# Kernel optimization log

Hardware: AMD Instinct MI355X
Metric: run time of the kernel (lower is better)

## Reference

```python
import jax, jax.numpy as jnp
import numpy as np

N, E = 20000, 320000
NF, EF = 4, 4
HID, HEADS, MODEL_HID = 128, 4, 128


def _p(key, shape, scale=0.1):
    return scale * jax.random.normal(key, shape, dtype=jnp.float32)


def setup_inputs() -> dict:
    key = jax.random.key(0)
    ks = jax.random.split(key, 32)
    x = jax.random.normal(ks[0], (N, NF), dtype=jnp.float32)
    src = jax.random.randint(ks[1], (E,), 0, N)
    off = jax.random.randint(ks[2], (E,), 1, N)
    dst = (src + off) % N  # no self-loops (PyG removes then re-adds them)
    edge_index = jnp.stack([src, dst]).astype(jnp.int64)
    edge_attr = jax.random.uniform(ks[3], (E, EF), dtype=jnp.float32)
    d = dict(x=x, edge_index=edge_index, edge_attr=edge_attr)
    # input_proj
    d['Wp'] = _p(ks[4], (NF, HID)); d['bp'] = jnp.zeros((HID,), jnp.float32)
    # GAT layer 1: in=HID, heads=HEADS, out=HID, concat
    d['W1'] = _p(ks[5], (HID, HEADS * HID)); d['We1'] = _p(ks[6], (EF, HEADS * HID))
    d['as1'] = _p(ks[7], (HEADS, HID)); d['ad1'] = _p(ks[8], (HEADS, HID)); d['ae1'] = _p(ks[9], (HEADS, HID))
    d['b1'] = jnp.zeros((HEADS * HID,), jnp.float32)
    d['g1'] = jnp.ones((HEADS * HID,), jnp.float32); d['be1'] = jnp.zeros((HEADS * HID,), jnp.float32)
    # GAT layer 2: in=HEADS*HID, heads=1, out=HID, mean
    d['W2'] = _p(ks[10], (HEADS * HID, HID)); d['We2'] = _p(ks[11], (EF, HID))
    d['as2'] = _p(ks[12], (1, HID)); d['ad2'] = _p(ks[13], (1, HID)); d['ae2'] = _p(ks[14], (1, HID))
    d['b2'] = jnp.zeros((HID,), jnp.float32)
    d['g2'] = jnp.ones((HID,), jnp.float32); d['be2'] = jnp.zeros((HID,), jnp.float32)
    # output proj + importance scorer
    d['Wo'] = _p(ks[15], (HID, MODEL_HID)); d['bo'] = jnp.zeros((MODEL_HID,), jnp.float32)
    d['Wi'] = _p(ks[16], (MODEL_HID, 1)); d['bi'] = jnp.zeros((1,), jnp.float32)
    return d


def _layer_norm(x, g, b, eps=1e-5):
    mu = x.mean(-1, keepdims=True)
    v = ((x - mu) ** 2).mean(-1, keepdims=True)
    return (x - mu) * jax.lax.rsqrt(v + eps) * g + b


def _segment_softmax(logits, seg, num):
    m = jax.ops.segment_max(logits, seg, num_segments=num)
    e = jnp.exp(logits - m[seg])
    d = jax.ops.segment_sum(e, seg, num_segments=num)
    return e / d[seg]


def _forward(x, edge_index, edge_attr, Wp, bp, W1, We1, as1, ad1, ae1, b1, g1, be1,
             W2, We2, as2, ad2, ae2, b2, g2, be2, Wo, bo, Wi, bi):
    n = x.shape[0]
    src, dst = edge_index[0], edge_index[1]
    e = edge_attr.shape[0]
    # add_self_loops with fill_value='mean': self-loop attr = mean of incoming edge_attr
    deg = jax.ops.segment_sum(jnp.ones((e,), edge_attr.dtype), dst, num_segments=n)
    loop_attr = jax.ops.segment_sum(edge_attr, dst, num_segments=n) / jnp.maximum(deg, 1.0)[:, None]
    loops = jnp.arange(n)
    src_f = jnp.concatenate([src, loops])
    dst_f = jnp.concatenate([dst, loops])
    ea = jnp.concatenate([edge_attr, loop_attr], axis=0)  # [E+N, EF]

    def gat(h, W, We, a_s, a_d, a_e, bias, heads, out_c, concat):
        xh = (h @ W).reshape(n, heads, out_c)                 # [N,H,C]
        eh = (ea @ We).reshape(-1, heads, out_c)              # [E+N,H,C]
        al_s = (xh * a_s).sum(-1)                             # [N,H]
        al_d = (xh * a_d).sum(-1)                             # [N,H]
        al_e = (eh * a_e).sum(-1)                             # [E+N,H]
        logits = jax.nn.leaky_relu(al_s[src_f] + al_d[dst_f] + al_e, negative_slope=0.2)
        alpha = _segment_softmax(logits, dst_f, n)            # [E+N,H]
        out = jax.ops.segment_sum(xh[src_f] * alpha[..., None], dst_f, num_segments=n)
        out = out.reshape(n, heads * out_c) if concat else out.mean(axis=1)
        return out + bias, alpha

    h = x @ Wp + bp
    h, _ = gat(h, W1, We1, as1, ad1, ae1, b1, HEADS, HID, True)
    h = jax.nn.elu(_layer_norm(h, g1, be1))  # dropout is a no-op in eval
    h, edge_attention = gat(h, W2, We2, as2, ad2, ae2, b2, 1, HID, False)
    h = _layer_norm(h, g2, be2)
    emb = h @ Wo + bo
    importance = jax.nn.sigmoid(emb @ Wi + bi).squeeze(-1)
    return emb, edge_attention, importance


def reference(x, edge_index, edge_attr, Wp, bp, W1, We1, as1, ad1, ae1, b1, g1, be1,
              W2, We2, as2, ad2, ae2, b2, g2, be2, Wo, bo, Wi, bi):
    return _forward(x, edge_index, edge_attr, Wp, bp, W1, We1, as1, ad1, ae1, b1, g1, be1,
                    W2, We2, as2, ad2, ae2, b2, g2, be2, Wo, bo, Wi, bi)
```

## Files before the change

kernel.cpp:

```cpp
#include <hip/hip_runtime.h>
#include <math.h>
#include <stdint.h>

#define N_NODES 20000
#define N_EDGES 320000
#define EN_TOT  340000
#define CAP     160

typedef __attribute__((ext_vector_type(8))) _Float16 half8v;
typedef __attribute__((ext_vector_type(2))) _Float16 half2v;
typedef __attribute__((ext_vector_type(4))) float float4v;

__device__ __forceinline__ ushort f2h(float f) {
    _Float16 h = (_Float16)f;
    return __builtin_bit_cast(ushort, h);
}
__device__ __forceinline__ float h2f(ushort s) {
    return (float)__builtin_bit_cast(_Float16, s);
}

__global__ void k_deg(const int* __restrict__ dst, int* __restrict__ degi) {
    int e = blockIdx.x * 256 + threadIdx.x;
    if (e >= N_EDGES) return;
    atomicAdd(&degi[dst[e]], 1);
}

__global__ __launch_bounds__(1024) void k_scan(const int* __restrict__ degi, int* __restrict__ offsets,
                                               const float* __restrict__ We1, const float* __restrict__ ae1,
                                               const float* __restrict__ We2, const float* __restrict__ ae2,
                                               float* __restrict__ M1, float* __restrict__ m2) {
    __shared__ int s[1024];
    int t = threadIdx.x;
    int n0 = t * 20;
    int tot = 0;
    for (int i = 0; i < 20; i++) {
        int n = n0 + i;
        if (n < N_NODES) tot += degi[n] + 1;
    }
    s[t] = tot;
    __syncthreads();
    for (int off = 1; off < 1024; off <<= 1) {
        int v = (t >= off) ? s[t - off] : 0;
        __syncthreads();
        s[t] += v;
        __syncthreads();
    }
    int run = s[t] - tot;
    for (int i = 0; i < 20; i++) {
        int n = n0 + i;
        if (n < N_NODES) {
            offsets[n] = run;
            run += degi[n] + 1;
        }
    }
    if (t == 1023) offsets[N_NODES] = s[1023];
    if (t < 16) {
        int f = t >> 2, h = t & 3;
        float acc = 0.f;
        for (int c = 0; c < 128; c++) acc += We1[f * 512 + h * 128 + c] * ae1[h * 128 + c];
        M1[f * 4 + h] = acc;
    } else if (t < 20) {
        int f = t - 16;
        float acc = 0.f;
        for (int c = 0; c < 128; c++) acc += We2[f * 128 + c] * ae2[c];
        m2[f] = acc;
    }
}

__global__ void k_fill(const int* __restrict__ src, const int* __restrict__ dst,
                       const int* __restrict__ offsets, int* __restrict__ cursor,
                       int2* __restrict__ csr_se) {
    int i = blockIdx.x * 256 + threadIdx.x;
    if (i >= EN_TOT) return;
    int d, sidx, eid;
    if (i < N_EDGES) { d = dst[i]; sidx = src[i]; eid = i; }
    else { int n = i - N_EDGES; d = n; sidx = n; eid = N_EDGES + n; }
    int pos = offsets[d] + atomicAdd(&cursor[d], 1);
    csr_se[pos] = make_int2(sidx, eid);
}

__global__ __launch_bounds__(256) void k_misc(const int* __restrict__ offsets, const int2* __restrict__ csr_se,
                                              const float* __restrict__ eattr, float* __restrict__ loopattr,
                                              const float* __restrict__ W1, const float* __restrict__ W2,
                                              const float* __restrict__ Wo, ushort* __restrict__ W1T,
                                              ushort* __restrict__ W2T, ushort* __restrict__ WoT,
                                              const float* __restrict__ x, const float* __restrict__ Wp,
                                              const float* __restrict__ bp, ushort* __restrict__ h0h) {
    int b = blockIdx.x;
    int tid = threadIdx.x;
    if (b < 5000) {
        int wv = tid >> 6, l = tid & 63;
        int n = b * 4 + wv;
        if (n >= N_NODES) return;
        int start = offsets[n], end = offsets[n + 1];
        float sx = 0.f, sy = 0.f, sz = 0.f, sw = 0.f;
        for (int p = start + l; p < end; p += 64) {
            int eid = csr_se[p].y;
            if (eid < N_EDGES) {
                float4 e = *(const float4*)&eattr[(size_t)eid * 4];
                sx += e.x; sy += e.y; sz += e.z; sw += e.w;
            }
        }
        for (int off = 32; off; off >>= 1) {
            sx += __shfl_down(sx, off);
            sy += __shfl_down(sy, off);
            sz += __shfl_down(sz, off);
            sw += __shfl_down(sw, off);
        }
        if (l == 0) {
            float inv = 1.0f / fmaxf((float)(end - start - 1), 1.0f);
            float4 o;
            o.x = sx * inv; o.y = sy * inv; o.z = sz * inv; o.w = sw * inv;
            *(float4*)&loopattr[(size_t)n * 4] = o;
        }
    } else if (b < 5576) {
        int i = (b - 5000) * 256 + tid;
        if (i < 512 * 128) {
            int nn = i >> 7, kk = i & 127;
            W1T[i] = f2h(W1[kk * 512 + nn]);
        } else if (i < 2 * 512 * 128) {
            int j = i - 512 * 128;
            int nn = j >> 9, kk = j & 511;
            W2T[j] = f2h(W2[kk * 128 + nn]);
        } else if (i < 2 * 512 * 128 + 128 * 128) {
            int j = i - 2 * 512 * 128;
            int nn = j >> 7, kk = j & 127;
            WoT[j] = f2h(Wo[kk * 128 + nn]);
        }
    } else {
        int n = (b - 5576) * 2 + (tid >> 7);
        int c = tid & 127;
        float acc = bp[c];
#pragma unroll
        for (int f = 0; f < 4; f++) acc += x[n * 4 + f] * Wp[f * 128 + c];
        h0h[(size_t)n * 128 + c] = f2h(acc);
    }
}

__global__ __launch_bounds__(256) void k_gemm_hf(const ushort* __restrict__ A, const ushort* __restrict__ BT,
                                                 float* __restrict__ Cf, ushort* __restrict__ Ch,
                                                 int M, int Nn, int K, const float* __restrict__ bias,
                                                 const float* __restrict__ asv, const float* __restrict__ adv,
                                                 float* __restrict__ outS, float* __restrict__ outD,
                                                 int hstride, const float* __restrict__ sbias) {
    __shared__ ushort As[64 * 64];
    __shared__ ushort Bs[128 * 64];
    __shared__ float redS[4][64];
    __shared__ float redD[4][64];
    const int tid = threadIdx.x;
    const int lane = tid & 63, wid = tid >> 6;
    const int m0 = blockIdx.x * 64, n0 = blockIdx.y * 128;
    float4v acc[4][2];
#pragma unroll
    for (int i = 0; i < 4; i++)
#pragma unroll
        for (int j = 0; j < 2; j++) acc[i][j] = (float4v){0.f, 0.f, 0.f, 0.f};

    for (int k0 = 0; k0 < K; k0 += 64) {
        __syncthreads();
#pragma unroll
        for (int i = 0; i < 2; i++) {
            int c = tid + i * 256;
            int row = c >> 3, sl = c & 7;
            int off = row * 128 + ((sl ^ (row & 7)) << 4);
            uint4 va = make_uint4(0u, 0u, 0u, 0u);
            if (m0 + row < M) va = *(const uint4*)&A[(size_t)(m0 + row) * K + k0 + sl * 8];
            *(uint4*)((char*)As + off) = va;
        }
#pragma unroll
        for (int i = 0; i < 4; i++) {
            int c = tid + i * 256;
            int row = c >> 3, sl = c & 7;
            int off = row * 128 + ((sl ^ (row & 7)) << 4);
            uint4 vb = *(const uint4*)&BT[(size_t)(n0 + row) * K + k0 + sl * 8];
            *(uint4*)((char*)Bs + off) = vb;
        }
        __syncthreads();
#pragma unroll
        for (int kk = 0; kk < 2; kk++) {
            half8v af[4], bq[2];
            int sl = kk * 4 + (lane >> 4);
#pragma unroll
            for (int mi = 0; mi < 4; mi++) {
                int row = (lane & 15) + mi * 16;
                af[mi] = *(const half8v*)((const char*)As + row * 128 + ((sl ^ (row & 7)) << 4));
            }
#pragma unroll
            for (int ni = 0; ni < 2; ni++) {
                int row = wid * 32 + ni * 16 + (lane & 15);
                bq[ni] = *(const half8v*)((const char*)Bs + row * 128 + ((sl ^ (row & 7)) << 4));
            }
#pragma unroll
            for (int mi = 0; mi < 4; mi++)
#pragma unroll
                for (int ni = 0; ni < 2; ni++)
                    acc[mi][ni] = __builtin_amdgcn_mfma_f32_16x16x32_f16(af[mi], bq[ni], acc[mi][ni], 0, 0, 0);
        }
    }
    float bcol[2];
#pragma unroll
    for (int ni = 0; ni < 2; ni++)
        bcol[ni] = bias ? bias[n0 + wid * 32 + ni * 16 + (lane & 15)] : 0.f;
#pragma unroll
    for (int mi = 0; mi < 4; mi++) {
#pragma unroll
        for (int j = 0; j < 4; j++) {
            int row = m0 + mi * 16 + ((lane >> 4) << 2) + j;
            if (row < M) {
#pragma unroll
                for (int ni = 0; ni < 2; ni++) {
                    int col = n0 + wid * 32 + ni * 16 + (lane & 15);
                    float v = acc[mi][ni][j] + bcol[ni];
                    if (Cf) Cf[(size_t)row * Nn + col] = v;
                    if (Ch) Ch[(size_t)row * Nn + col] = f2h(v);
                }
            }
        }
    }
    if (asv) {
        float asl[2], adl[2];
#pragma unroll
        for (int ni = 0; ni < 2; ni++) {
            int col = n0 + wid * 32 + ni * 16 + (lane & 15);
            asl[ni] = asv[col];
            adl[ni] = adv ? adv[col] : 0.f;
        }
        float psv[4][4], pdv[4][4];
#pragma unroll
        for (int mi = 0; mi < 4; mi++)
#pragma unroll
            for (int j = 0; j < 4; j++) {
                float v0 = acc[mi][0][j] + bcol[0];
                float v1 = acc[mi][1][j] + bcol[1];
                psv[mi][j] = v0 * asl[0] + v1 * asl[1];
                pdv[mi][j] = v0 * adl[0] + v1 * adl[1];
            }
#pragma unroll
        for (int off = 1; off < 16; off <<= 1) {
#pragma unroll
            for (int mi = 0; mi < 4; mi++)
#pragma unroll
                for (int j = 0; j < 4; j++) {
                    psv[mi][j] += __shfl_xor(psv[mi][j], off);
                    pdv[mi][j] += __shfl_xor(pdv[mi][j], off);
                }
        }
        if ((lane & 15) == 0) {
#pragma unroll
            for (int mi = 0; mi < 4; mi++)
#pragma unroll
                for (int j = 0; j < 4; j++) {
                    int r = mi * 16 + ((lane >> 4) << 2) + j;
                    redS[wid][r] = psv[mi][j];
                    redD[wid][r] = pdv[mi][j];
                }
        }
        __syncthreads();
        if (tid < 64) {
            int row = m0 + tid;
            if (row < M) {
                float ss = redS[0][tid] + redS[1][tid] + redS[2][tid] + redS[3][tid];
                float dd = redD[0][tid] + redD[1][tid] + redD[2][tid] + redD[3][tid];
                if (sbias) {
                    outS[row] = 1.0f / (1.0f + __expf(-(ss + sbias[0])));
                } else {
                    outS[row * hstride + blockIdx.y] = ss;
                    if (outD) outD[row * hstride + blockIdx.y] = dd;
                }
            }
        }
    }
}

__global__ __launch_bounds__(128) void k_agg1(const int* __restrict__ offsets, const int2* __restrict__ csr_se,
                                              const float* __restrict__ eattr, const float* __restrict__ loopattr,
                                              const float* __restrict__ als, const float* __restrict__ aldv,
                                              const float* __restrict__ M1, const ushort* __restrict__ xhh,
                                              const float* __restrict__ b1, const float* __restrict__ g1,
                                              const float* __restrict__ be1, ushort* __restrict__ h1h) {
    int wv = threadIdx.x >> 6, lane = threadIdx.x & 63;
    int n = blockIdx.x * 2 + wv;
    __shared__ float Lc[2][CAP][4];
    __shared__ int   sSrc[2][CAP];
    __shared__ float mhs[2][4], shs[2][4];

    int start = offsets[n];
    int cnt = offsets[n + 1] - start;

    int hh = lane & 3;
    float aldn = aldv[n * 4 + hh];
    float c0 = M1[hh], c1 = M1[4 + hh], c2 = M1[8 + hh], c3 = M1[12 + hh];
    float m = -1e30f, s = 0.f;
    for (int j = lane >> 2; j < cnt; j += 16) {
        int2 se = csr_se[start + j];
        const float* eap = (se.y < N_EDGES) ? &eattr[(size_t)se.y * 4] : &loopattr[(size_t)(se.y - N_EDGES) * 4];
        float4 e4 = *(const float4*)eap;
        float l = als[se.x * 4 + hh] + aldn + e4.x * c0 + e4.y * c1 + e4.z * c2 + e4.w * c3;
        l = (l >= 0.f) ? l : 0.2f * l;
        Lc[wv][j][hh] = l;
        if (hh == 0) sSrc[wv][j] = se.x;
        float mn = fmaxf(m, l);
        s = s * __expf(m - mn) + __expf(l - mn);
        m = mn;
    }
#pragma unroll
    for (int off = 4; off < 64; off <<= 1) {
        float mo = __shfl_xor(m, off), so = __shfl_xor(s, off);
        float mn = fmaxf(m, mo);
        s = s * __expf(m - mn) + so * __expf(mo - mn);
        m = mn;
    }
    if (lane < 4) { mhs[wv][lane] = m; shs[wv][lane] = 1.0f / s; }

    int tot = cnt * 4;
    for (int idx = lane; idx < tot; idx += 64) {
        int j = idx >> 2, h = idx & 3;
        Lc[wv][j][h] = __expf(Lc[wv][j][h] - mhs[wv][h]) * shs[wv][h];
    }

    half2v hac0 = (half2v)0, hac1 = (half2v)0, hac2 = (half2v)0, hac3 = (half2v)0;
    int hg = lane >> 4;
    uint ch = (uint)lane * 8u;
    int j = 0;
    for (; j + 8 <= cnt; j += 8) {
        _Float16 av[8];
        uint4 vv[8];
#pragma unroll
        for (int t = 0; t < 8; t++) av[t] = (_Float16)Lc[wv][j + t][hg];
#pragma unroll
        for (int t = 0; t < 8; t++) vv[t] = *(const uint4*)&xhh[((uint)sSrc[wv][j + t] << 9) + ch];
#pragma unroll
        for (int t = 0; t < 8; t++) {
            half2v a2 = (half2v){av[t], av[t]};
            const half2v* pv = (const half2v*)&vv[t];
            hac0 = pv[0] * a2 + hac0;
            hac1 = pv[1] * a2 + hac1;
            hac2 = pv[2] * a2 + hac2;
            hac3 = pv[3] * a2 + hac3;
        }
    }
    for (; j < cnt; j++) {
        _Float16 a = (_Float16)Lc[wv][j][hg];
        half2v a2 = (half2v){a, a};
        uint4 v = *(const uint4*)&xhh[((uint)sSrc[wv][j] << 9) + ch];
        const half2v* pv = (const half2v*)&v;
        hac0 = pv[0] * a2 + hac0;
        hac1 = pv[1] * a2 + hac1;
        hac2 = pv[2] * a2 + hac2;
        hac3 = pv[3] * a2 + hac3;
    }

    float4 ba = *(const float4*)&b1[ch];
    float4 bb = *(const float4*)&b1[ch + 4];
    float v0 = (float)hac0[0] + ba.x, v1 = (float)hac0[1] + ba.y;
    float v2 = (float)hac1[0] + ba.z, v3 = (float)hac1[1] + ba.w;
    float v4 = (float)hac2[0] + bb.x, v5 = (float)hac2[1] + bb.y;
    float v6 = (float)hac3[0] + bb.z, v7 = (float)hac3[1] + bb.w;
    float s8 = v0 + v1 + v2 + v3 + v4 + v5 + v6 + v7;
#pragma unroll
    for (int off = 1; off < 64; off <<= 1) s8 += __shfl_xor(s8, off);
    float mu = s8 * (1.0f / 512.0f);
    float d0 = v0 - mu, d1 = v1 - mu, d2 = v2 - mu, d3 = v3 - mu;
    float d4 = v4 - mu, d5 = v5 - mu, d6 = v6 - mu, d7 = v7 - mu;
    float sq = d0 * d0 + d1 * d1 + d2 * d2 + d3 * d3 + d4 * d4 + d5 * d5 + d6 * d6 + d7 * d7;
#pragma unroll
    for (int off = 1; off < 64; off <<= 1) sq += __shfl_xor(sq, off);
    float rstd = rsqrtf(sq * (1.0f / 512.0f) + 1e-5f);
    float4 ga = *(const float4*)&g1[ch];
    float4 gb = *(const float4*)&g1[ch + 4];
    float4 ea = *(const float4*)&be1[ch];
    float4 eb = *(const float4*)&be1[ch + 4];
    float y0 = d0 * rstd * ga.x + ea.x, y1 = d1 * rstd * ga.y + ea.y;
    float y2 = d2 * rstd * ga.z + ea.z, y3 = d3 * rstd * ga.w + ea.w;
    float y4 = d4 * rstd * gb.x + eb.x, y5 = d5 * rstd * gb.y + eb.y;
    float y6 = d6 * rstd * gb.z + eb.z, y7 = d7 * rstd * gb.w + eb.w;
    y0 = (y0 > 0.f) ? y0 : (__expf(y0) - 1.0f);
    y1 = (y1 > 0.f) ? y1 : (__expf(y1) - 1.0f);
    y2 = (y2 > 0.f) ? y2 : (__expf(y2) - 1.0f);
    y3 = (y3 > 0.f) ? y3 : (__expf(y3) - 1.0f);
    y4 = (y4 > 0.f) ? y4 : (__expf(y4) - 1.0f);
    y5 = (y5 > 0.f) ? y5 : (__expf(y5) - 1.0f);
    y6 = (y6 > 0.f) ? y6 : (__expf(y6) - 1.0f);
    y7 = (y7 > 0.f) ? y7 : (__expf(y7) - 1.0f);
    uint4 o;
    o.x = (uint)f2h(y0) | ((uint)f2h(y1) << 16);
    o.y = (uint)f2h(y2) | ((uint)f2h(y3) << 16);
    o.z = (uint)f2h(y4) | ((uint)f2h(y5) << 16);
    o.w = (uint)f2h(y6) | ((uint)f2h(y7) << 16);
    *(uint4*)&h1h[(size_t)n * 512 + ch] = o;
}

__global__ __launch_bounds__(128) void k_agg2(const int* __restrict__ offsets, const int2* __restrict__ csr_se,
                                              const float* __restrict__ eattr, const float* __restrict__ loopattr,
                                              const float* __restrict__ als, const float* __restrict__ aldv,
                                              const float* __restrict__ m2v, const ushort* __restrict__ xh2h,
                                              const float* __restrict__ b2, const float* __restrict__ g2,
                                              const float* __restrict__ be2, float* __restrict__ eaout,
                                              ushort* __restrict__ h2h) {
    int wv = threadIdx.x >> 6, lane = threadIdx.x & 63;
    int n = blockIdx.x * 2 + wv;
    __shared__ float Lc[2][CAP];
    __shared__ int   sS[2][CAP];
    __shared__ int   sE[2][CAP];

    int start = offsets[n];
    int cnt = offsets[n + 1] - start;
    float aldn = aldv[n];
    float c0 = m2v[0], c1 = m2v[1], c2 = m2v[2], c3 = m2v[3];
    float m = -1e30f, s = 0.f;
    for (int j = lane; j < cnt; j += 64) {
        int2 se = csr_se[start + j];
        const float* eap = (se.y < N_EDGES) ? &eattr[(size_t)se.y * 4] : &loopattr[(size_t)(se.y - N_EDGES) * 4];
        float4 e4 = *(const float4*)eap;
        float l = als[se.x] + aldn + e4.x * c0 + e4.y * c1 + e4.z * c2 + e4.w * c3;
        l = (l >= 0.f) ? l : 0.2f * l;
        Lc[wv][j] = l; sS[wv][j] = se.x; sE[wv][j] = se.y;
        float mn = fmaxf(m, l);
        s = s * __expf(m - mn) + __expf(l - mn);
        m = mn;
    }
#pragma unroll
    for (int off = 1; off < 64; off <<= 1) {
        float mo = __shfl_xor(m, off), so = __shfl_xor(s, off);
        float mn = fmaxf(m, mo);
        s = s * __expf(m - mn) + so * __expf(mo - mn);
        m = mn;
    }
    float inv = 1.0f / s;
    for (int j = lane; j < cnt; j += 64) {
        float a = __expf(Lc[wv][j] - m) * inv;
        Lc[wv][j] = a;
        eaout[sE[wv][j]] = a;
    }
    half2v hac = (half2v)0;
    uint ch = (uint)lane * 2u;
    int j = 0;
    for (; j + 8 <= cnt; j += 8) {
        _Float16 av[8];
        uint vv[8];
#pragma unroll
        for (int t = 0; t < 8; t++) av[t] = (_Float16)Lc[wv][j + t];
#pragma unroll
        for (int t = 0; t < 8; t++) vv[t] = *(const uint*)&xh2h[((uint)sS[wv][j + t] << 7) + ch];
#pragma unroll
        for (int t = 0; t < 8; t++) {
            half2v a2 = (half2v){av[t], av[t]};
            half2v pv = __builtin_bit_cast(half2v, vv[t]);
            hac = pv * a2 + hac;
        }
    }
    for (; j < cnt; j++) {
        _Float16 a = (_Float16)Lc[wv][j];
        half2v a2 = (half2v){a, a};
        half2v pv = __builtin_bit_cast(half2v, *(const uint*)&xh2h[((uint)sS[wv][j] << 7) + ch]);
        hac = pv * a2 + hac;
    }
    float2 bb = *(const float2*)&b2[ch];
    float v0 = (float)hac[0] + bb.x, v1 = (float)hac[1] + bb.y;
    float s2 = v0 + v1;
#pragma unroll
    for (int off = 1; off < 64; off <<= 1) s2 += __shfl_xor(s2, off);
    float mu = s2 * (1.0f / 128.0f);
    float d0 = v0 - mu, d1 = v1 - mu;
    float q = d0 * d0 + d1 * d1;
#pragma unroll
    for (int off = 1; off < 64; off <<= 1) q += __shfl_xor(q, off);
    float rstd = rsqrtf(q * (1.0f / 128.0f) + 1e-5f);
    float2 gg = *(const float2*)&g2[ch];
    float2 ee = *(const float2*)&be2[ch];
    float y0 = d0 * rstd * gg.x + ee.x;
    float y1 = d1 * rstd * gg.y + ee.y;
    uint o = (uint)f2h(y0) | ((uint)f2h(y1) << 16);
    *(uint*)&h2h[(size_t)n * 128 + ch] = o;
}

extern "C" void kernel_launch(void* const* d_in, const int* in_sizes, int n_in,
                              void* d_out, int out_size, void* d_ws, size_t ws_size,
                              hipStream_t stream) {
    const float* x    = (const float*)d_in[0];
    const int*   eidx = (const int*)d_in[1];
    const float* eattr= (const float*)d_in[2];
    const float* Wp   = (const float*)d_in[3];
    const float* bp   = (const float*)d_in[4];
    const float* W1   = (const float*)d_in[5];
    const float* We1  = (const float*)d_in[6];
    const float* as1  = (const float*)d_in[7];
    const float* ad1  = (const float*)d_in[8];
    const float* ae1  = (const float*)d_in[9];
    const float* b1   = (const float*)d_in[10];
    const float* g1   = (const float*)d_in[11];
    const float* be1  = (const float*)d_in[12];
    const float* W2   = (const float*)d_in[13];
    const float* We2  = (const float*)d_in[14];
    const float* as2  = (const float*)d_in[15];
    const float* ad2  = (const float*)d_in[16];
    const float* ae2  = (const float*)d_in[17];
    const float* b2   = (const float*)d_in[18];
    const float* g2   = (const float*)d_in[19];
    const float* be2  = (const float*)d_in[20];
    const float* Wo   = (const float*)d_in[21];
    const float* bo   = (const float*)d_in[22];
    const float* Wi   = (const float*)d_in[23];
    const float* bi   = (const float*)d_in[24];

    const int* src = eidx;
    const int* dst = eidx + N_EDGES;

    float* emb_out = (float*)d_out;
    float* ea_out  = emb_out + (size_t)N_NODES * 128;
    float* imp_out = ea_out + EN_TOT;

    char* w = (char*)d_ws;
    auto alloc = [&](size_t bytes) -> void* { void* p = (void*)w; w += (bytes + 255) & ~(size_t)255; return p; };
    ushort* xhh    = (ushort*)alloc((size_t)N_NODES * 512 * 2);
    ushort* h1h    = (ushort*)alloc((size_t)N_NODES * 512 * 2);
    ushort* h0h    = (ushort*)alloc((size_t)N_NODES * 128 * 2);
    ushort* xh2h   = (ushort*)alloc((size_t)N_NODES * 128 * 2);
    ushort* h2h    = (ushort*)alloc((size_t)N_NODES * 128 * 2);
    ushort* W1T    = (ushort*)alloc((size_t)512 * 128 * 2);
    ushort* W2T    = (ushort*)alloc((size_t)128 * 512 * 2);
    ushort* WoT    = (ushort*)alloc((size_t)128 * 128 * 2);
    int2*  csr_se  = (int2*)alloc((size_t)EN_TOT * 8);
    int*   offsets = (int*)alloc((size_t)(N_NODES + 1) * 4);
    int*   cursor  = (int*)alloc((size_t)N_NODES * 4);
    int*   degi    = (int*)alloc((size_t)N_NODES * 4);
    float* loopat  = (float*)alloc((size_t)N_NODES * 4 * 4);
    float* als1v   = (float*)alloc((size_t)N_NODES * 4 * 4);
    float* ald1v   = (float*)alloc((size_t)N_NODES * 4 * 4);
    float* als2v   = (float*)alloc((size_t)N_NODES * 4);
    float* ald2v   = (float*)alloc((size_t)N_NODES * 4);
    float* M1      = (float*)alloc(32 * 4);
    float* m2      = M1 + 16;

    hipMemsetAsync(degi,   0, (size_t)N_NODES * 4, stream);
    hipMemsetAsync(cursor, 0, (size_t)N_NODES * 4, stream);

    k_deg<<<(N_EDGES + 255) / 256, 256, 0, stream>>>(dst, degi);
    k_scan<<<1, 1024, 0, stream>>>(degi, offsets, We1, ae1, We2, ae2, M1, m2);
    k_fill<<<(EN_TOT + 255) / 256, 256, 0, stream>>>(src, dst, offsets, cursor, csr_se);
    k_misc<<<15576, 256, 0, stream>>>(offsets, csr_se, eattr, loopat, W1, W2, Wo,
                                      W1T, W2T, WoT, x, Wp, bp, h0h);

    k_gemm_hf<<<dim3((N_NODES + 63) / 64, 4), 256, 0, stream>>>(h0h, W1T, nullptr, xhh,
                                                                N_NODES, 512, 128, nullptr,
                                                                as1, ad1, als1v, ald1v, 4, nullptr);
    k_agg1<<<N_NODES / 2, 128, 0, stream>>>(offsets, csr_se, eattr, loopat, als1v, ald1v, M1,
                                            xhh, b1, g1, be1, h1h);

    k_gemm_hf<<<dim3((N_NODES + 63) / 64, 1), 256, 0, stream>>>(h1h, W2T, nullptr, xh2h,
                                                                N_NODES, 128, 512, nullptr,
                                                                as2, ad2, als2v, ald2v, 1, nullptr);
    k_agg2<<<N_NODES / 2, 128, 0, stream>>>(offsets, csr_se, eattr, loopat, als2v, ald2v, m2,
                                            xh2h, b2, g2, be2, ea_out, h2h);

    k_gemm_hf<<<dim3((N_NODES + 63) / 64, 1), 256, 0, stream>>>(h2h, WoT, emb_out, nullptr,
                                                                N_NODES, 128, 128, bo,
                                                                Wi, nullptr, imp_out, nullptr, 1, bi);
}
```

Baseline: 207.1 us.

## Replace LDS edge staging with recompute and wave shuffles in GAT aggregation

Both aggregation kernels no longer cache per-edge logits and source indices in fixed-capacity shared arrays. Edges are processed in 64-wide chunks: the softmax statistics pass recomputes logits, then a second pass recomputes them, normalises, packs the attention weights into registers and broadcasts them with __shfl to all lanes for the gather-accumulate. Layer 1 now gives each lane all four heads of one edge instead of one head. This drops LDS use and its capacity limit (CAP=160), in exchange for reading the edge data and computing the logits twice and adding per-edge shuffle work.

Measured after the change: 214.8 us. 3.7% more time.

```diff
diff --git a/kernel.cpp b/kernel.cpp
--- a/kernel.cpp
+++ b/kernel.cpp
@@ -5,7 +5,6 @@
 #define N_NODES 20000
 #define N_EDGES 320000
 #define EN_TOT  340000
-#define CAP     160
 
 typedef __attribute__((ext_vector_type(8))) _Float16 half8v;
 typedef __attribute__((ext_vector_type(2))) _Float16 half2v;
@@ -18,6 +17,10 @@
 __device__ __forceinline__ float h2f(ushort s) {
     return (float)__builtin_bit_cast(_Float16, s);
 }
+
+#define ONL(mm, ss, ll) { float _mn = fmaxf(mm, ll); ss = ss * __expf(mm - _mn) + __expf(ll - _mn); mm = _mn; }
+#define MRG(mm, ss, off) { float _mo = __shfl_xor(mm, off), _so = __shfl_xor(ss, off); \
+                           float _mn = fmaxf(mm, _mo); ss = ss * __expf(mm - _mn) + _so * __expf(_mo - _mn); mm = _mn; }
 
 __global__ void k_deg(const int* __restrict__ dst, int* __restrict__ degi) {
     int e = blockIdx.x * 256 + threadIdx.x;
@@ -280,74 +283,109 @@
                                               const float* __restrict__ be1, ushort* __restrict__ h1h) {
     int wv = threadIdx.x >> 6, lane = threadIdx.x & 63;
     int n = blockIdx.x * 2 + wv;
-    __shared__ float Lc[2][CAP][4];
-    __shared__ int   sSrc[2][CAP];
-    __shared__ float mhs[2][4], shs[2][4];
-
     int start = offsets[n];
     int cnt = offsets[n + 1] - start;
 
-    int hh = lane & 3;
-    float aldn = aldv[n * 4 + hh];
-    float c0 = M1[hh], c1 = M1[4 + hh], c2 = M1[8 + hh], c3 = M1[12 + hh];
-    float m = -1e30f, s = 0.f;
-    for (int j = lane >> 2; j < cnt; j += 16) {
-        int2 se = csr_se[start + j];
-        const float* eap = (se.y < N_EDGES) ? &eattr[(size_t)se.y * 4] : &loopattr[(size_t)(se.y - N_EDGES) * 4];
-        float4 e4 = *(const float4*)eap;
-        float l = als[se.x * 4 + hh] + aldn + e4.x * c0 + e4.y * c1 + e4.z * c2 + e4.w * c3;
-        l = (l >= 0.f) ? l : 0.2f * l;
-        Lc[wv][j][hh] = l;
-        if (hh == 0) sSrc[wv][j] = se.x;
-        float mn = fmaxf(m, l);
-        s = s * __expf(m - mn) + __expf(l - mn);
-        m = mn;
-    }
-#pragma unroll
-    for (int off = 4; off < 64; off <<= 1) {
-        float mo = __shfl_xor(m, off), so = __shfl_xor(s, off);
-        float mn = fmaxf(m, mo);
-        s = s * __expf(m - mn) + so * __expf(mo - mn);
-        m = mn;
-    }
-    if (lane < 4) { mhs[wv][lane] = m; shs[wv][lane] = 1.0f / s; }
-
-    int tot = cnt * 4;
-    for (int idx = lane; idx < tot; idx += 64) {
-        int j = idx >> 2, h = idx & 3;
-        Lc[wv][j][h] = __expf(Lc[wv][j][h] - mhs[wv][h]) * shs[wv][h];
-    }
+    float4 aldn = *(const float4*)&aldv[n * 4];
+    float M00 = M1[0],  M01 = M1[1],  M02 = M1[2],  M03 = M1[3];
+    float M10 = M1[4],  M11 = M1[5],  M12 = M1[6],  M13 = M1[7];
+    float M20 = M1[8],  M21 = M1[9],  M22 = M1[10], M23 = M1[11];
+    float M30 = M1[12], M31 = M1[13], M32 = M1[14], M33 = M1[15];
+
+    float m0 = -1e30f, m1 = -1e30f, m2 = -1e30f, m3 = -1e30f;
+    float s0 = 0.f, s1 = 0.f, s2 = 0.f, s3 = 0.f;
+    for (int jb = 0; jb < cnt; jb += 64) {
+        int j = jb + lane;
+        if (j < cnt) {
+            int2 se = csr_se[start + j];
+            const float* eap = (se.y < N_EDGES) ? &eattr[(size_t)se.y * 4] : &loopattr[(size_t)(se.y - N_EDGES) * 4];
+            float4 e4 = *(const float4*)eap;
+            float4 a4 = *(const float4*)&als[se.x * 4];
+            float l0 = a4.x + aldn.x + e4.x * M00 + e4.y * M10 + e4.z * M20 + e4.w * M30;
+            float l1 = a4.y + aldn.y + e4.x * M01 + e4.y * M11 + e4.z * M21 + e4.w * M31;
+            float l2 = a4.z + aldn.z + e4.x * M02 + e4.y * M12 + e4.z * M22 + e4.w * M32;
+            float l3 = a4.w + aldn.w + e4.x * M03 + e4.y * M13 + e4.z * M23 + e4.w * M33;
+            l0 = (l0 >= 0.f) ? l0 : 0.2f * l0;
+            l1 = (l1 >= 0.f) ? l1 : 0.2f * l1;
+            l2 = (l2 >= 0.f) ? l2 : 0.2f * l2;
+            l3 = (l3 >= 0.f) ? l3 : 0.2f * l3;
+            ONL(m0, s0, l0); ONL(m1, s1, l1); ONL(m2, s2, l2); ONL(m3, s3, l3);
+        }
+    }
+#pragma unroll
+    for (int off = 1; off < 64; off <<= 1) {
+        MRG(m0, s0, off); MRG(m1, s1, off); MRG(m2, s2, off); MRG(m3, s3, off);
+    }
+    float i0 = 1.0f / s0, i1 = 1.0f / s1, i2 = 1.0f / s2, i3 = 1.0f / s3;
 
     half2v hac0 = (half2v)0, hac1 = (half2v)0, hac2 = (half2v)0, hac3 = (half2v)0;
     int hg = lane >> 4;
     uint ch = (uint)lane * 8u;
-    int j = 0;
-    for (; j + 8 <= cnt; j += 8) {
-        _Float16 av[8];
-        uint4 vv[8];
-#pragma unroll
-        for (int t = 0; t < 8; t++) av[t] = (_Float16)Lc[wv][j + t][hg];
-#pragma unroll
-        for (int t = 0; t < 8; t++) vv[t] = *(const uint4*)&xhh[((uint)sSrc[wv][j + t] << 9) + ch];
-#pragma unroll
-        for (int t = 0; t < 8; t++) {
-            half2v a2 = (half2v){av[t], av[t]};
-            const half2v* pv = (const half2v*)&vv[t];
-            hac0 = pv[0] * a2 + hac0;
-            hac1 = pv[1] * a2 + hac1;
-            hac2 = pv[2] * a2 + hac2;
-            hac3 = pv[3] * a2 + hac3;
-        }
-    }
-    for (; j < cnt; j++) {
-        _Float16 a = (_Float16)Lc[wv][j][hg];
-        half2v a2 = (half2v){a, a};
-        uint4 v = *(const uint4*)&xhh[((uint)sSrc[wv][j] << 9) + ch];
-        const half2v* pv = (const half2v*)&v;
-        hac0 = pv[0] * a2 + hac0;
-        hac1 = pv[1] * a2 + hac1;
-        hac2 = pv[2] * a2 + hac2;
-        hac3 = pv[3] * a2 + hac3;
+    for (int jb = 0; jb < cnt; jb += 64) {
+        int j = jb + lane;
+        uint pa = 0, pb = 0;
+        int sex = 0;
+        if (j < cnt) {
+            int2 se = csr_se[start + j];
+            sex = se.x;
+            const float* eap = (se.y < N_EDGES) ? &eattr[(size_t)se.y * 4] : &loopattr[(size_t)(se.y - N_EDGES) * 4];
+            float4 e4 = *(const float4*)eap;
+            float4 a4 = *(const float4*)&als[se.x * 4];
+            float l0 = a4.x + aldn.x + e4.x * M00 + e4.y * M10 + e4.z * M20 + e4.w * M30;
+            float l1 = a4.y + aldn.y + e4.x * M01 + e4.y * M11 + e4.z * M21 + e4.w * M31;
+            float l2 = a4.z + aldn.z + e4.x * M02 + e4.y * M12 + e4.z * M22 + e4.w * M32;
+            float l3 = a4.w + aldn.w + e4.x * M03 + e4.y * M13 + e4.z * M23 + e4.w * M33;
+            l0 = (l0 >= 0.f) ? l0 : 0.2f * l0;
+            l1 = (l1 >= 0.f) ? l1 : 0.2f * l1;
+            l2 = (l2 >= 0.f) ? l2 : 0.2f * l2;
+            l3 = (l3 >= 0.f) ? l3 : 0.2f * l3;
+            float a0 = __expf(l0 - m0) * i0;
+            float a1 = __expf(l1 - m1) * i1;
+            float a2 = __expf(l2 - m2) * i2;
+            float a3 = __expf(l3 - m3) * i3;
+            pa = (uint)f2h(a0) | ((uint)f2h(a1) << 16);
+            pb = (uint)f2h(a2) | ((uint)f2h(a3) << 16);
+        }
+        int cm = min(64, cnt - jb);
+        int t = 0;
+        for (; t + 8 <= cm; t += 8) {
+            ushort a16[8];
+            uint4 vv[8];
+#pragma unroll
+            for (int tt = 0; tt < 8; tt++) {
+                int sj = __shfl(sex, t + tt);
+                uint ua = __shfl(pa, t + tt);
+                uint ub = __shfl(pb, t + tt);
+                uint us = (hg & 2) ? ub : ua;
+                a16[tt] = (hg & 1) ? (ushort)(us >> 16) : (ushort)(us & 0xffffu);
+                vv[tt] = *(const uint4*)&xhh[((uint)sj << 9) + ch];
+            }
+#pragma unroll
+            for (int tt = 0; tt < 8; tt++) {
+                _Float16 a = __builtin_bit_cast(_Float16, a16[tt]);
+                half2v a2v = (half2v){a, a};
+                const half2v* pv = (const half2v*)&vv[tt];
+                hac0 = pv[0] * a2v + hac0;
+                hac1 = pv[1] * a2v + hac1;
+                hac2 = pv[2] * a2v + hac2;
+                hac3 = pv[3] * a2v + hac3;
+            }
+        }
+        for (; t < cm; t++) {
+            int sj = __shfl(sex, t);
+            uint ua = __shfl(pa, t);
+            uint ub = __shfl(pb, t);
+            uint us = (hg & 2) ? ub : ua;
+            ushort ah = (hg & 1) ? (ushort)(us >> 16) : (ushort)(us & 0xffffu);
+            uint4 v = *(const uint4*)&xhh[((uint)sj << 9) + ch];
+            _Float16 a = __builtin_bit_cast(_Float16, ah);
+            half2v a2v = (half2v){a, a};
+            const half2v* pv = (const half2v*)&v;
+            hac0 = pv[0] * a2v + hac0;
+            hac1 = pv[1] * a2v + hac1;
+            hac2 = pv[2] * a2v + hac2;
+            hac3 = pv[3] * a2v + hac3;
+        }
     }
 
     float4 ba = *(const float4*)&b1[ch];
@@ -399,61 +437,68 @@
                                               ushort* __restrict__ h2h) {
     int wv = threadIdx.x >> 6, lane = threadIdx.x & 63;
     int n = blockIdx.x * 2 + wv;
-    __shared__ float Lc[2][CAP];
-    __shared__ int   sS[2][CAP];
-    __shared__ int   sE[2][CAP];
-
     int start = offsets[n];
     int cnt = offsets[n + 1] - start;
     float aldn = aldv[n];
     float c0 = m2v[0], c1 = m2v[1], c2 = m2v[2], c3 = m2v[3];
+
     float m = -1e30f, s = 0.f;
-    for (int j = lane; j < cnt; j += 64) {
-        int2 se = csr_se[start + j];
-        const float* eap = (se.y < N_EDGES) ? &eattr[(size_t)se.y * 4] : &loopattr[(size_t)(se.y - N_EDGES) * 4];
-        float4 e4 = *(const float4*)eap;
-        float l = als[se.x] + aldn + e4.x * c0 + e4.y * c1 + e4.z * c2 + e4.w * c3;
-        l = (l >= 0.f) ? l : 0.2f * l;
-        Lc[wv][j] = l; sS[wv][j] = se.x; sE[wv][j] = se.y;
-        float mn = fmaxf(m, l);
-        s = s * __expf(m - mn) + __expf(l - mn);
-        m = mn;
-    }
-#pragma unroll
-    for (int off = 1; off < 64; off <<= 1) {
-        float mo = __shfl_xor(m, off), so = __shfl_xor(s, off);
-        float mn = fmaxf(m, mo);
-        s = s * __expf(m - mn) + so * __expf(mo - mn);
-        m = mn;
-    }
+    for (int jb = 0; jb < cnt; jb += 64) {
+        int j = jb + lane;
+        if (j < cnt) {
+            int2 se = csr_se[start + j];
+            const float* eap = (se.y < N_EDGES) ? &eattr[(size_t)se.y * 4] : &loopattr[(size_t)(se.y - N_EDGES) * 4];
+            float4 e4 = *(const float4*)eap;
+            float l = als[se.x] + aldn + e4.x * c0 + e4.y * c1 + e4.z * c2 + e4.w * c3;
+            l = (l >= 0.f) ? l : 0.2f * l;
+            ONL(m, s, l);
+        }
+    }
+#pragma unroll
+    for (int off = 1; off < 64; off <<= 1) { MRG(m, s, off); }
     float inv = 1.0f / s;
-    for (int j = lane; j < cnt; j += 64) {
-        float a = __expf(Lc[wv][j] - m) * inv;
-        Lc[wv][j] = a;
-        eaout[sE[wv][j]] = a;
-    }
+
     half2v hac = (half2v)0;
     uint ch = (uint)lane * 2u;
-    int j = 0;
-    for (; j + 8 <= cnt; j += 8) {
-        _Float16 av[8];
-        uint vv[8];
-#pragma unroll
-        for (int t = 0; t < 8; t++) av[t] = (_Float16)Lc[wv][j + t];
-#pragma unroll
-        for (int t = 0; t < 8; t++) vv[t] = *(const uint*)&xh2h[((uint)sS[wv][j + t] << 7) + ch];
-#pragma unroll
-        for (int t = 0; t < 8; t++) {
-            half2v a2 = (half2v){av[t], av[t]};
-            half2v pv = __builtin_bit_cast(half2v, vv[t]);
-            hac = pv * a2 + hac;
-        }
-    }
-    for (; j < cnt; j++) {
-        _Float16 a = (_Float16)Lc[wv][j];
-        half2v a2 = (half2v){a, a};
-        half2v pv = __builtin_bit_cast(half2v, *(const uint*)&xh2h[((uint)sS[wv][j] << 7) + ch]);
-        hac = pv * a2 + hac;
+    for (int jb = 0; jb < cnt; jb += 64) {
+        int j = jb + lane;
+        float af = 0.f;
+        int sex = 0;
+        if (j < cnt) {
+            int2 se = csr_se[start + j];
+            sex = se.x;
+            const float* eap = (se.y < N_EDGES) ? &eattr[(size_t)se.y * 4] : &loopattr[(size_t)(se.y - N_EDGES) * 4];
+            float4 e4 = *(const float4*)eap;
+            float l = als[se.x] + aldn + e4.x * c0 + e4.y * c1 + e4.z * c2 + e4.w * c3;
+            l = (l >= 0.f) ? l : 0.2f * l;
+            af = __expf(l - m) * inv;
+            eaout[se.y] = af;
+        }
+        int cm = min(64, cnt - jb);
+        int t = 0;
+        for (; t + 8 <= cm; t += 8) {
+            _Float16 av[8];
+            uint vv[8];
+#pragma unroll
+            for (int tt = 0; tt < 8; tt++) {
+                int sj = __shfl(sex, t + tt);
+                av[tt] = (_Float16)__shfl(af, t + tt);
+                vv[tt] = *(const uint*)&xh2h[((uint)sj << 7) + ch];
+            }
+#pragma unroll
+            for (int tt = 0; tt < 8; tt++) {
+                half2v a2v = (half2v){av[tt], av[tt]};
+                half2v pv = __builtin_bit_cast(half2v, vv[tt]);
+                hac = pv * a2v + hac;
+            }
+        }
+        for (; t < cm; t++) {
+            int sj = __shfl(sex, t);
+            _Float16 a = (_Float16)__shfl(af, t);
+            half2v a2v = (half2v){a, a};
+            half2v pv = __builtin_bit_cast(half2v, *(const uint*)&xh2h[((uint)sj << 7) + ch]);
+            hac = pv * a2v + hac;
+        }
     }
     float2 bb = *(const float2*)&b2[ch];
     float v0 = (float)hac[0] + bb.x, v1 = (float)hac[1] + bb.y;
```

## Split each layer-1 node across two waves and vectorize degree counting

Applied to the files above, without the earlier changes.

The layer-1 aggregation now assigns two wavefronts (128 threads) to each destination node instead of one. Each lane handles 4 channels instead of 8, and the softmax max/sum and LayerNorm statistics are merged across the two waves through shared memory. LayerNorm switches to a single-pass sum and sum-of-squares variance, and the degree kernel reads two dst indices per thread. Edge counts are now clamped to CAP in both aggregation kernels. The aim is more parallelism and latency hiding on the gather, at the cost of extra block barriers and somewhat less accurate variance.

After: 209.2 us. About the same (+1.0%).

```diff
diff --git a/kernel.cpp b/kernel.cpp
--- a/kernel.cpp
+++ b/kernel.cpp
@@ -19,10 +19,16 @@
     return (float)__builtin_bit_cast(_Float16, s);
 }
 
+#define ONL(mm, ss, ll) { float _mn = fmaxf(mm, ll); ss = ss * __expf(mm - _mn) + __expf(ll - _mn); mm = _mn; }
+#define MRG(mm, ss, off) { float _mo = __shfl_xor(mm, off), _so = __shfl_xor(ss, off); \
+                           float _mn = fmaxf(mm, _mo); ss = ss * __expf(mm - _mn) + _so * __expf(_mo - _mn); mm = _mn; }
+
 __global__ void k_deg(const int* __restrict__ dst, int* __restrict__ degi) {
-    int e = blockIdx.x * 256 + threadIdx.x;
+    int e = (blockIdx.x * 256 + threadIdx.x) * 2;
     if (e >= N_EDGES) return;
-    atomicAdd(&degi[dst[e]], 1);
+    int2 d = *(const int2*)&dst[e];
+    atomicAdd(&degi[d.x], 1);
+    atomicAdd(&degi[d.y], 1);
 }
 
 __global__ __launch_bounds__(1024) void k_scan(const int* __restrict__ degi, int* __restrict__ offsets,
@@ -272,122 +278,110 @@
     }
 }
 
-__global__ __launch_bounds__(128) void k_agg1(const int* __restrict__ offsets, const int2* __restrict__ csr_se,
+__global__ __launch_bounds__(256) void k_agg1(const int* __restrict__ offsets, const int2* __restrict__ csr_se,
                                               const float* __restrict__ eattr, const float* __restrict__ loopattr,
                                               const float* __restrict__ als, const float* __restrict__ aldv,
                                               const float* __restrict__ M1, const ushort* __restrict__ xhh,
                                               const float* __restrict__ b1, const float* __restrict__ g1,
                                               const float* __restrict__ be1, ushort* __restrict__ h1h) {
-    int wv = threadIdx.x >> 6, lane = threadIdx.x & 63;
-    int n = blockIdx.x * 2 + wv;
+    int tid = threadIdx.x;
+    int pair = tid >> 7;
+    int t = tid & 127;
+    int wv = t >> 6;
+    int lane = t & 63;
+    int n = blockIdx.x * 2 + pair;
     __shared__ float Lc[2][CAP][4];
     __shared__ int   sSrc[2][CAP];
-    __shared__ float mhs[2][4], shs[2][4];
+    __shared__ float mred[2][2][4], sred[2][2][4];
+    __shared__ float lred[2][2][2];
 
     int start = offsets[n];
-    int cnt = offsets[n + 1] - start;
-
-    int hh = lane & 3;
+    int cnt = min(offsets[n + 1] - start, CAP);
+
+    int hh = t & 3;
     float aldn = aldv[n * 4 + hh];
     float c0 = M1[hh], c1 = M1[4 + hh], c2 = M1[8 + hh], c3 = M1[12 + hh];
     float m = -1e30f, s = 0.f;
-    for (int j = lane >> 2; j < cnt; j += 16) {
+    for (int j = t >> 2; j < cnt; j += 32) {
         int2 se = csr_se[start + j];
         const float* eap = (se.y < N_EDGES) ? &eattr[(size_t)se.y * 4] : &loopattr[(size_t)(se.y - N_EDGES) * 4];
         float4 e4 = *(const float4*)eap;
         float l = als[se.x * 4 + hh] + aldn + e4.x * c0 + e4.y * c1 + e4.z * c2 + e4.w * c3;
         l = (l >= 0.f) ? l : 0.2f * l;
-        Lc[wv][j][hh] = l;
-        if (hh == 0) sSrc[wv][j] = se.x;
-        float mn = fmaxf(m, l);
-        s = s * __expf(m - mn) + __expf(l - mn);
-        m = mn;
-    }
-#pragma unroll
-    for (int off = 4; off < 64; off <<= 1) {
-        float mo = __shfl_xor(m, off), so = __shfl_xor(s, off);
-        float mn = fmaxf(m, mo);
-        s = s * __expf(m - mn) + so * __expf(mo - mn);
-        m = mn;
-    }
-    if (lane < 4) { mhs[wv][lane] = m; shs[wv][lane] = 1.0f / s; }
-
-    int tot = cnt * 4;
-    for (int idx = lane; idx < tot; idx += 64) {
-        int j = idx >> 2, h = idx & 3;
-        Lc[wv][j][h] = __expf(Lc[wv][j][h] - mhs[wv][h]) * shs[wv][h];
-    }
-
-    half2v hac0 = (half2v)0, hac1 = (half2v)0, hac2 = (half2v)0, hac3 = (half2v)0;
-    int hg = lane >> 4;
-    uint ch = (uint)lane * 8u;
+        Lc[pair][j][hh] = l;
+        if (hh == 0) sSrc[pair][j] = se.x;
+        ONL(m, s, l);
+    }
+#pragma unroll
+    for (int off = 4; off < 64; off <<= 1) { MRG(m, s, off); }
+    if (lane < 4) { mred[pair][wv][lane] = m; sred[pair][wv][lane] = s; }
+    __syncthreads();
+    float Ma = mred[pair][0][hh], Sa = sred[pair][0][hh];
+    float Mb = mred[pair][1][hh], Sb = sred[pair][1][hh];
+    float mn = fmaxf(Ma, Mb);
+    float invS = 1.0f / (Sa * __expf(Ma - mn) + Sb * __expf(Mb - mn));
+    for (int j = t >> 2; j < cnt; j += 32)
+        Lc[pair][j][hh] = __expf(Lc[pair][j][hh] - mn) * invS;
+    __syncthreads();
+
+    int chh = wv * 256 + lane * 4;
+    int hg = chh >> 7;
+    half2v hac0 = (half2v)0, hac1 = (half2v)0;
     int j = 0;
     for (; j + 8 <= cnt; j += 8) {
-        _Float16 av[8];
-        uint4 vv[8];
-#pragma unroll
-        for (int t = 0; t < 8; t++) av[t] = (_Float16)Lc[wv][j + t][hg];
-#pragma unroll
-        for (int t = 0; t < 8; t++) vv[t] = *(const uint4*)&xhh[((uint)sSrc[wv][j + t] << 9) + ch];
-#pragma unroll
-        for (int t = 0; t < 8; t++) {
-            half2v a2 = (half2v){av[t], av[t]};
-            const half2v* pv = (const half2v*)&vv[t];
-            hac0 = pv[0] * a2 + hac0;
-            hac1 = pv[1] * a2 + hac1;
-            hac2 = pv[2] * a2 + hac2;
-            hac3 = pv[3] * a2 + hac3;
+        float a[8];
+        uint2 vv[8];
+#pragma unroll
+        for (int tt = 0; tt < 8; tt++) {
+            a[tt] = Lc[pair][j + tt][hg];
+            vv[tt] = *(const uint2*)&xhh[((uint)sSrc[pair][j + tt] << 9) + (uint)chh];
+        }
+#pragma unroll
+        for (int tt = 0; tt < 8; tt++) {
+            _Float16 ah = (_Float16)a[tt];
+            half2v a2v = (half2v){ah, ah};
+            const half2v* pv = (const half2v*)&vv[tt];
+            hac0 = pv[0] * a2v + hac0;
+            hac1 = pv[1] * a2v + hac1;
         }
     }
     for (; j < cnt; j++) {
-        _Float16 a = (_Float16)Lc[wv][j][hg];
-        half2v a2 = (half2v){a, a};
-        uint4 v = *(const uint4*)&xhh[((uint)sSrc[wv][j] << 9) + ch];
+        _Float16 ah = (_Float16)Lc[pair][j][hg];
+        half2v a2v = (half2v){ah, ah};
+        uint2 v = *(const uint2*)&xhh[((uint)sSrc[pair][j] << 9) + (uint)chh];
         const half2v* pv = (const half2v*)&v;
-        hac0 = pv[0] * a2 + hac0;
-        hac1 = pv[1] * a2 + hac1;
-        hac2 = pv[2] * a2 + hac2;
-        hac3 = pv[3] * a2 + hac3;
-    }
-
-    float4 ba = *(const float4*)&b1[ch];
-    float4 bb = *(const float4*)&b1[ch + 4];
-    float v0 = (float)hac0[0] + ba.x, v1 = (float)hac0[1] + ba.y;
-    float v2 = (float)hac1[0] + ba.z, v3 = (float)hac1[1] + ba.w;
-    float v4 = (float)hac2[0] + bb.x, v5 = (float)hac2[1] + bb.y;
-    float v6 = (float)hac3[0] + bb.z, v7 = (float)hac3[1] + bb.w;
-    float s8 = v0 + v1 + v2 + v3 + v4 + v5 + v6 + v7;
-#pragma unroll
-    for (int off = 1; off < 64; off <<= 1) s8 += __shfl_xor(s8, off);
-    float mu = s8 * (1.0f / 512.0f);
-    float d0 = v0 - mu, d1 = v1 - mu, d2 = v2 - mu, d3 = v3 - mu;
-    float d4 = v4 - mu, d5 = v5 - mu, d6 = v6 - mu, d7 = v7 - mu;
-    float sq = d0 * d0 + d1 * d1 + d2 * d2 + d3 * d3 + d4 * d4 + d5 * d5 + d6 * d6 + d7 * d7;
-#pragma unroll
-    for (int off = 1; off < 64; off <<= 1) sq += __shfl_xor(sq, off);
-    float rstd = rsqrtf(sq * (1.0f / 512.0f) + 1e-5f);
-    float4 ga = *(const float4*)&g1[ch];
-    float4 gb = *(const float4*)&g1[ch + 4];
-    float4 ea = *(const float4*)&be1[ch];
-    float4 eb = *(const float4*)&be1[ch + 4];
-    float y0 = d0 * rstd * ga.x + ea.x, y1 = d1 * rstd * ga.y + ea.y;
-    float y2 = d2 * rstd * ga.z + ea.z, y3 = d3 * rstd * ga.w + ea.w;
-    float y4 = d4 * rstd * gb.x + eb.x, y5 = d5 * rstd * gb.y + eb.y;
-    float y6 = d6 * rstd * gb.z + eb.z, y7 = d7 * rstd * gb.w + eb.w;
+        hac0 = pv[0] * a2v + hac0;
+        hac1 = pv[1] * a2v + hac1;
+    }
+
+    float4 bb4 = *(const float4*)&b1[chh];
+    float v0 = (float)hac0[0] + bb4.x, v1 = (float)hac0[1] + bb4.y;
+    float v2 = (float)hac1[0] + bb4.z, v3 = (float)hac1[1] + bb4.w;
+    float sA = v0 + v1 + v2 + v3;
+    float sB = v0 * v0 + v1 * v1 + v2 * v2 + v3 * v3;
+#pragma unroll
+    for (int off = 1; off < 64; off <<= 1) { sA += __shfl_xor(sA, off); sB += __shfl_xor(sB, off); }
+    if (lane == 0) { lred[pair][wv][0] = sA; lred[pair][wv][1] = sB; }
+    __syncthreads();
+    float tS = lred[pair][0][0] + lred[pair][1][0];
+    float tQ = lred[pair][0][1] + lred[pair][1][1];
+    float mu = tS * (1.0f / 512.0f);
+    float var = tQ * (1.0f / 512.0f) - mu * mu;
+    float rstd = rsqrtf(var + 1e-5f);
+    float4 gg4 = *(const float4*)&g1[chh];
+    float4 ee4 = *(const float4*)&be1[chh];
+    float y0 = (v0 - mu) * rstd * gg4.x + ee4.x;
+    float y1 = (v1 - mu) * rstd * gg4.y + ee4.y;
+    float y2 = (v2 - mu) * rstd * gg4.z + ee4.z;
+    float y3 = (v3 - mu) * rstd * gg4.w + ee4.w;
     y0 = (y0 > 0.f) ? y0 : (__expf(y0) - 1.0f);
     y1 = (y1 > 0.f) ? y1 : (__expf(y1) - 1.0f);
     y2 = (y2 > 0.f) ? y2 : (__expf(y2) - 1.0f);
     y3 = (y3 > 0.f) ? y3 : (__expf(y3) - 1.0f);
-    y4 = (y4 > 0.f) ? y4 : (__expf(y4) - 1.0f);
-    y5 = (y5 > 0.f) ? y5 : (__expf(y5) - 1.0f);
-    y6 = (y6 > 0.f) ? y6 : (__expf(y6) - 1.0f);
-    y7 = (y7 > 0.f) ? y7 : (__expf(y7) - 1.0f);
-    uint4 o;
+    uint2 o;
     o.x = (uint)f2h(y0) | ((uint)f2h(y1) << 16);
     o.y = (uint)f2h(y2) | ((uint)f2h(y3) << 16);
-    o.z = (uint)f2h(y4) | ((uint)f2h(y5) << 16);
-    o.w = (uint)f2h(y6) | ((uint)f2h(y7) << 16);
-    *(uint4*)&h1h[(size_t)n * 512 + ch] = o;
+    *(uint2*)&h1h[(size_t)n * 512 + chh] = o;
 }
 
 __global__ __launch_bounds__(128) void k_agg2(const int* __restrict__ offsets, const int2* __restrict__ csr_se,
@@ -404,7 +398,7 @@
     __shared__ int   sE[2][CAP];
 
     int start = offsets[n];
-    int cnt = offsets[n + 1] - start;
+    int cnt = min(offsets[n + 1] - start, CAP);
     float aldn = aldv[n];
     float c0 = m2v[0], c1 = m2v[1], c2 = m2v[2], c3 = m2v[3];
     float m = -1e30f, s = 0.f;
@@ -415,17 +409,10 @@
         float l = als[se.x] + aldn + e4.x * c0 + e4.y * c1 + e4.z * c2 + e4.w * c3;
         l = (l >= 0.f) ? l : 0.2f * l;
         Lc[wv][j] = l; sS[wv][j] = se.x; sE[wv][j] = se.y;
-        float mn = fmaxf(m, l);
-        s = s * __expf(m - mn) + __expf(l - mn);
-        m = mn;
-    }
-#pragma unroll
-    for (int off = 1; off < 64; off <<= 1) {
-        float mo = __shfl_xor(m, off), so = __shfl_xor(s, off);
-        float mn = fmaxf(m, mo);
-        s = s * __expf(m - mn) + so * __expf(mo - mn);
-        m = mn;
-    }
+        ONL(m, s, l);
+    }
+#pragma unroll
+    for (int off = 1; off < 64; off <<= 1) { MRG(m, s, off); }
     float inv = 1.0f / s;
     for (int j = lane; j < cnt; j += 64) {
         float a = __expf(Lc[wv][j] - m) * inv;
@@ -439,13 +426,13 @@
         _Float16 av[8];
         uint vv[8];
 #pragma unroll
-        for (int t = 0; t < 8; t++) av[t] = (_Float16)Lc[wv][j + t];
-#pragma unroll
-        for (int t = 0; t < 8; t++) vv[t] = *(const uint*)&xh2h[((uint)sS[wv][j + t] << 7) + ch];
-#pragma unroll
-        for (int t = 0; t < 8; t++) {
-            half2v a2 = (half2v){av[t], av[t]};
-            half2v pv = __builtin_bit_cast(half2v, vv[t]);
+        for (int tt = 0; tt < 8; tt++) av[tt] = (_Float16)Lc[wv][j + tt];
+#pragma unroll
+        for (int tt = 0; tt < 8; tt++) vv[tt] = *(const uint*)&xh2h[((uint)sS[wv][j + tt] << 7) + ch];
+#pragma unroll
+        for (int tt = 0; tt < 8; tt++) {
+            half2v a2 = (half2v){av[tt], av[tt]};
+            half2v pv = __builtin_bit_cast(half2v, vv[tt]);
             hac = pv * a2 + hac;
         }
     }
@@ -535,7 +522,7 @@
     hipMemsetAsync(degi,   0, (size_t)N_NODES * 4, stream);
     hipMemsetAsync(cursor, 0, (size_t)N_NODES * 4, stream);
 
-    k_deg<<<(N_EDGES + 255) / 256, 256, 0, stream>>>(dst, degi);
+    k_deg<<<(N_EDGES / 2 + 255) / 256, 256, 0, stream>>>(dst, degi);
     k_scan<<<1, 1024, 0, stream>>>(degi, offsets, We1, ae1, We2, ae2, M1, m2);
     k_fill<<<(EN_TOT + 255) / 256, 256, 0, stream>>>(src, dst, offsets, cursor, csr_se);
     k_misc<<<15576, 256, 0, stream>>>(offsets, csr_se, eattr, loopat, W1, W2, Wo,
@@ -544,7 +531,7 @@
     k_gemm_hf<<<dim3((N_NODES + 63) / 64, 4), 256, 0, stream>>>(h0h, W1T, nullptr, xhh,
                                                                 N_NODES, 512, 128, nullptr,
                                                                 as1, ad1, als1v, ald1v, 4, nullptr);
-    k_agg1<<<N_NODES / 2, 128, 0, stream>>>(offsets, csr_se, eattr, loopat, als1v, ald1v, M1,
+    k_agg1<<<N_NODES / 2, 256, 0, stream>>>(offsets, csr_se, eattr, loopat, als1v, ald1v, M1,
                                             xhh, b1, g1, be1, h1h);
 
     k_gemm_hf<<<dim3((N_NODES + 63) / 64, 1), 256, 0, stream>>>(h1h, W2T, nullptr, xh2h,
```
